# Kernel tuning notes

Measured on AMD Instinct MI355X. Metric: run time of the kernel, lower is better.

## Reference

```python
import jax, jax.numpy as jnp
import numpy as np

K = 20
EPS = 1e-5


def _bn(x, g, b):
    # inference-mode BatchNorm with running_mean=0, running_var=1 (fresh init)
    return x * (g / jnp.sqrt(1.0 + EPS)) + b


def _lrelu(x):
    return jax.nn.leaky_relu(x, 0.2)


def _knn(x, k):
    # x: [B,N,D] -> idx [B,N,k] of nearest neighbors (includes self)
    sq = jnp.sum(x * x, axis=-1)                       # [B,N]
    inner = jnp.einsum('bnd,bmd->bnm', x, x)           # [B,N,N]
    dist = sq[:, :, None] - 2.0 * inner + sq[:, None, :]
    _, idx = jax.lax.top_k(-dist, k)
    return idx


def _edge_feat(x, k):
    # x: [B,N,D] -> [B,N,k,2D] = concat(neighbor - center, center)
    idx = _knn(x, k)
    nbr = jax.vmap(lambda xb, ib: xb[ib])(x, idx)      # [B,N,k,D]
    ctr = jnp.broadcast_to(x[:, :, None, :], nbr.shape)
    return jnp.concatenate([nbr - ctr, ctr], axis=-1)


def _edge_conv(x, W, g, b, k):
    # conv1x1 (no bias) + BN + LeakyReLU + max over neighbors
    f = _edge_feat(x, k)                               # [B,N,k,2D]
    h = jnp.einsum('bnkc,oc->bnko', f, W)
    return jnp.max(_lrelu(_bn(h, g, b)), axis=2)       # [B,N,out]


def setup_inputs() -> dict:
    key = jax.random.key(0)
    ks = jax.random.split(key, 12)
    B, N = 8, 4096
    num_classes = 5
    r = lambda k_, shape: jax.random.normal(k_, shape, jnp.float32) * 0.1
    return {
        'xyz': jax.random.normal(ks[0], (B, N, 3), jnp.float32),
        'W1': r(ks[1], (64, 6)),   'g1': jnp.ones((64,), jnp.float32),  'b1': jnp.zeros((64,), jnp.float32),
        'W2': r(ks[2], (64, 128)), 'g2': jnp.ones((64,), jnp.float32),  'b2': jnp.zeros((64,), jnp.float32),
        'W3': r(ks[3], (64, 128)), 'g3': jnp.ones((64,), jnp.float32),  'b3': jnp.zeros((64,), jnp.float32),
        'W4': r(ks[4], (128, 128)),'g4': jnp.ones((128,), jnp.float32), 'b4': jnp.zeros((128,), jnp.float32),
        'W5': r(ks[5], (1024, 320)),'g5': jnp.ones((1024,), jnp.float32),'b5': jnp.zeros((1024,), jnp.float32),
        'Wl1': r(ks[6], (512, 2048)),'g6': jnp.ones((512,), jnp.float32),'b6': jnp.zeros((512,), jnp.float32),
        'Wl2': r(ks[7], (256, 512)), 'bl2': jnp.zeros((256,), jnp.float32),
        'g7': jnp.ones((256,), jnp.float32), 'b7': jnp.zeros((256,), jnp.float32),
        'Wl3': r(ks[8], (num_classes, 256)), 'bl3': jnp.zeros((num_classes,), jnp.float32),
    }


def reference(xyz, W1, g1, b1, W2, g2, b2, W3, g3, b3, W4, g4, b4,
              W5, g5, b5, Wl1, g6, b6, Wl2, bl2, g7, b7, Wl3, bl3):
    B, N, _ = xyz.shape
    k = min(K, N - 1)
    x1 = _edge_conv(xyz, W1, g1, b1, k)                # [B,N,64]
    x2 = _edge_conv(x1, W2, g2, b2, k)                 # [B,N,64]
    x3 = _edge_conv(x2, W3, g3, b3, k)                 # [B,N,64]
    x4 = _edge_conv(x3, W4, g4, b4, k)                 # [B,N,128]
    xc = jnp.concatenate([x1, x2, x3, x4], axis=-1)    # [B,N,320]
    h = _lrelu(_bn(jnp.einsum('bnc,oc->bno', xc, W5), g5, b5))  # [B,N,1024]
    gmax = jnp.max(h, axis=1)
    gavg = jnp.mean(h, axis=1)
    gfeat = jnp.concatenate([gmax, gavg], axis=-1)     # [B,2048]
    y = _lrelu(_bn(gfeat @ Wl1.T, g6, b6))             # dropout = identity (eval)
    y = _lrelu(_bn(y @ Wl2.T + bl2, g7, b7))
    y = y @ Wl3.T + bl3                                # [B,num_classes]
    return jnp.broadcast_to(y[:, None, :], (B, N, y.shape[-1]))
```

## Files before the change

kernel.cpp:

```cpp
#include <hip/hip_runtime.h>


constexpr int NB  = 8;
constexpr int NPT = 4096;
constexpr int KNB = 20;

typedef _Float16 half8 __attribute__((ext_vector_type(8)));
typedef float f32x4 __attribute__((ext_vector_type(4)));

__device__ __forceinline__ unsigned int fmono(float f) {
  unsigned int u = __float_as_uint(f);
  return u ^ ((unsigned int)(((int)u) >> 31) | 0x80000000u);
}

__device__ __attribute__((noinline)) unsigned long long sort_row(int row, int n,
                                                                 int lane) {
  extern __shared__ char smem[];
  unsigned long long* buf = (unsigned long long*)smem + (size_t)row * 64;
  const unsigned long long INFK = ~0ull;
  unsigned long long a = (lane < n) ? buf[lane] : INFK;
#pragma unroll
  for (int k = 2; k <= 64; k <<= 1) {
#pragma unroll
    for (int j = k >> 1; j > 0; j >>= 1) {
      const bool tm = (((lane & k) == 0) == ((lane & j) == 0));
      const unsigned long long oa = __shfl_xor(a, j, 64);
      a = ((a < oa) == tm) ? a : oa;
    }
  }
  if (lane < 20) buf[lane] = a;
  return a;
}

__device__ __forceinline__ void sel_q(unsigned long long key, int base_r,
                                      int quad, int l15, int lane,
                                      unsigned long long& tau_r, int& cnt_r) {
  extern __shared__ char smem[];
  unsigned long long* bufB = (unsigned long long*)smem;
  bool pass = key < tau_r;
  unsigned long long m = __ballot(pass);
  if (m == 0) return;
  unsigned int seg = (unsigned int)(m >> (quad * 16)) & 0xFFFFu;
  int pc = __popc(seg);
  const unsigned long long needm = __ballot(cnt_r + pc > 64);
  if (needm != 0) {
#pragma unroll
    for (int q = 0; q < 4; ++q) {
      if ((needm >> (q * 16)) & 1ull) {
        const int nq = __shfl(cnt_r, q * 16, 64);
        const unsigned long long sv = sort_row(base_r + q * 4, nq, lane);
        const unsigned long long t19 = __shfl(sv, 19, 64);
        if (quad == q) { tau_r = t19; cnt_r = 20; }
      }
    }
    pass = key < tau_r;
    m = __ballot(pass);
    seg = (unsigned int)(m >> (quad * 16)) & 0xFFFFu;
    pc = __popc(seg);
  }
  if (pass) {
    const int off = __popc(seg & ((1u << l15) - 1u));
    bufB[(size_t)(base_r + quad * 4) * 64 + cnt_r + off] = key;
  }
  cnt_r += pc;
}

__global__ __launch_bounds__(256) void cvt_xyz(const float* __restrict__ xyz,
                                               float* __restrict__ x0) {
  const int t = blockIdx.x * 256 + threadIdx.x;
  float4 v;
  v.x = xyz[t * 3 + 0];
  v.y = xyz[t * 3 + 1];
  v.z = xyz[t * 3 + 2];
  v.w = 0.0f;
  *(float4*)(x0 + (size_t)t * 4) = v;
}

__global__ __launch_bounds__(256) void sqsplit(const float* __restrict__ x,
                                               float* __restrict__ sqo,
                                               unsigned short* __restrict__ xhi,
                                               unsigned short* __restrict__ xlo) {
  const int t = blockIdx.x * 256 + threadIdx.x;
  const int p = t >> 2, c = t & 3;
  const float* src = x + (size_t)p * 64 + c * 16;
  float s = 0.0f;
  unsigned short hb[16], lb[16];
#pragma unroll
  for (int e = 0; e < 16; e += 4) {
    const float4 v = *(const float4*)(src + e);
    const float vv[4] = {v.x, v.y, v.z, v.w};
#pragma unroll
    for (int u = 0; u < 4; ++u) {
      const float f = vv[u];
      s = fmaf(f, f, s);
      const _Float16 h = (_Float16)f;
      const _Float16 l = (_Float16)(f - (float)h);
      hb[e + u] = __builtin_bit_cast(unsigned short, h);
      lb[e + u] = __builtin_bit_cast(unsigned short, l);
    }
  }
  unsigned short* dh = xhi + (size_t)p * 64 + c * 16;
  unsigned short* dl = xlo + (size_t)p * 64 + c * 16;
  *(uint4*)dh = *(uint4*)hb;
  *(uint4*)(dh + 8) = *(uint4*)(hb + 8);
  *(uint4*)dl = *(uint4*)lb;
  *(uint4*)(dl + 8) = *(uint4*)(lb + 8);
  s += __shfl_xor(s, 1, 64);
  s += __shfl_xor(s, 2, 64);
  if (c == 0) sqo[p] = s;
}

__global__ __launch_bounds__(256, 4) void knn3(const float* __restrict__ x0,
                                               int* __restrict__ idxout) {
  const int b = blockIdx.y, i0 = blockIdx.x * 64;
  const int tid = threadIdx.x, w = tid >> 6, lane = tid & 63;
  const int l15 = lane & 15, quad = lane >> 4;
  const float* xb = x0 + (size_t)b * (NPT * 4);

  float xix[4], xiy[4], xiz[4];
#pragma unroll
  for (int r = 0; r < 4; ++r) {
    const float4 v =
        *(const float4*)(xb + (size_t)(i0 + w * 16 + quad * 4 + r) * 4);
    xix[r] = v.x;
    xiy[r] = v.y;
    xiz[r] = v.z;
  }

  unsigned long long tau[4] = {~0ull, ~0ull, ~0ull, ~0ull};
  int cnt[4] = {0, 0, 0, 0};

  for (int jt = 0; jt < NPT / 64; ++jt) {
    const int j0 = jt * 64;
    float4 xj[4];
#pragma unroll
    for (int nj = 0; nj < 4; ++nj)
      xj[nj] = *(const float4*)(xb + (size_t)(j0 + nj * 16 + l15) * 4);
#pragma unroll
    for (int r = 0; r < 4; ++r) {
#pragma unroll
      for (int nj = 0; nj < 4; ++nj) {
        const float dx = xj[nj].x - xix[r];
        const float dy = xj[nj].y - xiy[r];
        const float dz = xj[nj].z - xiz[r];
        const float dd = fmaf(dx, dx, fmaf(dy, dy, dz * dz));
        const unsigned long long key =
            ((unsigned long long)fmono(dd) << 32) |
            (unsigned int)(j0 + nj * 16 + l15);
        sel_q(key, w * 16 + r, quad, l15, lane, tau[r], cnt[r]);
      }
    }
  }
#pragma unroll
  for (int rw = 0; rw < 16; ++rw) {
    const int q = rw >> 2, r = rw & 3;
    const int nq = __shfl(cnt[r], q * 16, 64);
    const unsigned long long sv = sort_row(w * 16 + rw, nq, lane);
    const int i = i0 + w * 16 + rw;
    if (lane < 20)
      idxout[((size_t)(b * NPT + i)) * KNB + lane] = (int)(unsigned int)sv;
  }
}

__global__ __launch_bounds__(256, 4) void knn_mfma(
    const unsigned short* __restrict__ xhi16,
    const unsigned short* __restrict__ xlo16,
    const float* __restrict__ sqn, int* __restrict__ idxout) {
  const int b = blockIdx.y, i0 = blockIdx.x * 64;
  const int tid = threadIdx.x, w = tid >> 6, lane = tid & 63;
  const int l15 = lane & 15, quad = lane >> 4;

  const half8* Hb = (const half8*)(xhi16 + (size_t)b * NPT * 64);
  const half8* Lb = (const half8*)(xlo16 + (size_t)b * NPT * 64);
  const float* sqb = sqn + b * NPT;

  const int ia = i0 + w * 16 + l15;
  const half8 ah0 = Hb[(size_t)ia * 8 + quad];
  const half8 ah1 = Hb[(size_t)ia * 8 + 4 + quad];
  const half8 al0 = Lb[(size_t)ia * 8 + quad];
  const half8 al1 = Lb[(size_t)ia * 8 + 4 + quad];

  unsigned long long tau[4] = {~0ull, ~0ull, ~0ull, ~0ull};
  int cnt[4] = {0, 0, 0, 0};

  for (int jt = 0; jt < NPT / 64; ++jt) {
    const int j0 = jt * 64;
    float sq4[4];
#pragma unroll
    for (int nj = 0; nj < 4; ++nj) sq4[nj] = sqb[j0 + nj * 16 + l15];
    f32x4 acc[4];
#pragma unroll
    for (int nj = 0; nj < 4; ++nj) {
      const int jb = j0 + nj * 16 + l15;
      const half8 bh0 = Hb[(size_t)jb * 8 + quad];
      const half8 bh1 = Hb[(size_t)jb * 8 + 4 + quad];
      const half8 bl0 = Lb[(size_t)jb * 8 + quad];
      const half8 bl1 = Lb[(size_t)jb * 8 + 4 + quad];
      f32x4 a = {0.0f, 0.0f, 0.0f, 0.0f};
      a = __builtin_amdgcn_mfma_f32_16x16x32_f16(al0, bh0, a, 0, 0, 0);
      a = __builtin_amdgcn_mfma_f32_16x16x32_f16(al1, bh1, a, 0, 0, 0);
      a = __builtin_amdgcn_mfma_f32_16x16x32_f16(ah0, bl0, a, 0, 0, 0);
      a = __builtin_amdgcn_mfma_f32_16x16x32_f16(ah1, bl1, a, 0, 0, 0);
      a = __builtin_amdgcn_mfma_f32_16x16x32_f16(ah0, bh0, a, 0, 0, 0);
      a = __builtin_amdgcn_mfma_f32_16x16x32_f16(ah1, bh1, a, 0, 0, 0);
      acc[nj] = a;
    }
#pragma unroll
    for (int r = 0; r < 4; ++r) {
#pragma unroll
      for (int nj = 0; nj < 4; ++nj) {
        const float dd = fmaf(-2.0f, acc[nj][r], sq4[nj]);
        const unsigned long long key =
            ((unsigned long long)fmono(dd) << 32) |
            (unsigned int)(j0 + nj * 16 + l15);
        sel_q(key, w * 16 + r, quad, l15, lane, tau[r], cnt[r]);
      }
    }
  }
#pragma unroll
  for (int rw = 0; rw < 16; ++rw) {
    const int q = rw >> 2, r = rw & 3;
    const int nq = __shfl(cnt[r], q * 16, 64);
    const unsigned long long sv = sort_row(w * 16 + rw, nq, lane);
    const int i = i0 + w * 16 + rw;
    if (lane < 20)
      idxout[((size_t)(b * NPT + i)) * KNB + lane] = (int)(unsigned int)sv;
  }
}

template <int DIN, int DS, int COUT>
__global__ __launch_bounds__(256) void edge_kernel(
    const float* __restrict__ x, const int* __restrict__ idx,
    const float* __restrict__ W, const float* __restrict__ g,
    const float* __restrict__ bia, float* __restrict__ out) {
  constexpr int CG = COUT / 64;
  const int lane = threadIdx.x & 63;
  const int wglob = blockIdx.x * 4 + (threadIdx.x >> 6);
  const int n_lin = __builtin_amdgcn_readfirstlane(wglob / CG);
  const int cg = __builtin_amdgcn_readfirstlane(wglob % CG);
  const int b = n_lin >> 12;
  const int n = n_lin & (NPT - 1);
  const int c = cg * 64 + lane;

  const float* wrow = W + (size_t)c * (2 * DIN);
  const float invs = 1.0f / sqrtf(1.0f + 1e-5f);
  const float s = g[c] * invs;
  const float bias = bia[c];

  const float* xb = x + (size_t)b * (NPT * DS);
  const float* xi = xb + (size_t)n * DS;

  float wa[DIN];
  float base = 0.0f;
  if constexpr (DIN == 3) {
    wa[0] = wrow[0]; wa[1] = wrow[1]; wa[2] = wrow[2];
    const float wb0 = wrow[3], wb1 = wrow[4], wb2 = wrow[5];
    const float4 vi = *(const float4*)xi;
    base = (wb0 - wa[0]) * vi.x + (wb1 - wa[1]) * vi.y + (wb2 - wa[2]) * vi.z;
  } else {
#pragma unroll
    for (int d0 = 0; d0 < DIN; d0 += 4) {
      const float4 w4 = *(const float4*)(wrow + d0);
      wa[d0 + 0] = w4.x; wa[d0 + 1] = w4.y; wa[d0 + 2] = w4.z; wa[d0 + 3] = w4.w;
    }
#pragma unroll
    for (int d0 = 0; d0 < DIN; d0 += 4) {
      const float4 wb4 = *(const float4*)(wrow + DIN + d0);
      const float4 v0 = *(const float4*)(xi + d0);
      base += (wb4.x - wa[d0 + 0]) * v0.x + (wb4.y - wa[d0 + 1]) * v0.y +
              (wb4.z - wa[d0 + 2]) * v0.z + (wb4.w - wa[d0 + 3]) * v0.w;
    }
  }
  base = s * base + bias;

  const int* ip = idx + (size_t)n_lin * KNB;
  float m = -3.0e38f;
  for (int k = 0; k < KNB; ++k) {
    const int j = __builtin_amdgcn_readfirstlane(ip[k]);
    const float* xj = xb + (size_t)j * DS;
    float acc = 0.0f;
    if constexpr (DIN == 3) {
      const float4 v = *(const float4*)xj;
      acc = wa[0] * v.x + wa[1] * v.y + wa[2] * v.z;
    } else {
#pragma unroll
      for (int d0 = 0; d0 < DIN; d0 += 8) {
        const float4 v0 = *(const float4*)(xj + d0);
        const float4 v1 = *(const float4*)(xj + d0 + 4);
        acc += wa[d0 + 0] * v0.x + wa[d0 + 1] * v0.y + wa[d0 + 2] * v0.z +
               wa[d0 + 3] * v0.w + wa[d0 + 4] * v1.x + wa[d0 + 5] * v1.y +
               wa[d0 + 6] * v1.z + wa[d0 + 7] * v1.w;
      }
    }
    float v = s * acc + base;
    v = v > 0.0f ? v : 0.2f * v;
    m = fmaxf(m, v);
  }
  out[(size_t)n_lin * COUT + c] = m;
}

__global__ __launch_bounds__(256) void conv5_kernel(
    const float* __restrict__ x1, const float* __restrict__ x2,
    const float* __restrict__ x3, const float* __restrict__ x4,
    const float* __restrict__ W5, const float* __restrict__ g5,
    const float* __restrict__ b5, float* __restrict__ pmax,
    float* __restrict__ psum) {
  __shared__ float xcT[320][32];
  __shared__ float wT[8][256];
  const int nb = blockIdx.x, cb = blockIdx.y, b = blockIdx.z;
  const int tid = threadIdx.x;
  const int n0 = nb * 32;

#pragma unroll
  for (int p = 0; p < 10; ++p) {
    const int q = tid + p * 256;
    const int nloc = q / 80;
    const int kg = (q % 80) * 4;
    const float* src;
    int koff;
    if (kg < 64)       { src = x1 + ((size_t)(b * NPT + n0 + nloc)) * 64;  koff = kg; }
    else if (kg < 128) { src = x2 + ((size_t)(b * NPT + n0 + nloc)) * 64;  koff = kg - 64; }
    else if (kg < 192) { src = x3 + ((size_t)(b * NPT + n0 + nloc)) * 64;  koff = kg - 128; }
    else               { src = x4 + ((size_t)(b * NPT + n0 + nloc)) * 128; koff = kg - 192; }
    const float4 v = *(const float4*)(src + koff);
    xcT[kg + 0][nloc] = v.x; xcT[kg + 1][nloc] = v.y;
    xcT[kg + 2][nloc] = v.z; xcT[kg + 3][nloc] = v.w;
  }

  const int cg = tid >> 2, ng = tid & 3;
  const int c0 = cg * 4, n0t = ng * 8;
  float acc[4][8];
#pragma unroll
  for (int r = 0; r < 4; ++r)
#pragma unroll
    for (int e = 0; e < 8; ++e) acc[r][e] = 0.0f;

  for (int kt = 0; kt < 40; ++kt) {
    __syncthreads();
    {
      const float* wsrc = W5 + (size_t)(cb * 256 + tid) * 320 + kt * 8;
      const float4 a = *(const float4*)wsrc;
      const float4 b4 = *(const float4*)(wsrc + 4);
      wT[0][tid] = a.x; wT[1][tid] = a.y; wT[2][tid] = a.z; wT[3][tid] = a.w;
      wT[4][tid] = b4.x; wT[5][tid] = b4.y; wT[6][tid] = b4.z; wT[7][tid] = b4.w;
    }
    __syncthreads();
#pragma unroll
    for (int kk = 0; kk < 8; ++kk) {
      const float4 w4 = *(const float4*)&wT[kk][c0];
      const float4 xa = *(const float4*)&xcT[kt * 8 + kk][n0t];
      const float4 xb4 = *(const float4*)&xcT[kt * 8 + kk][n0t + 4];
      const float wr[4] = {w4.x, w4.y, w4.z, w4.w};
      const float xr[8] = {xa.x, xa.y, xa.z, xa.w, xb4.x, xb4.y, xb4.z, xb4.w};
#pragma unroll
      for (int r = 0; r < 4; ++r)
#pragma unroll
        for (int e = 0; e < 8; ++e) acc[r][e] = fmaf(wr[r], xr[e], acc[r][e]);
    }
  }

  const float invs = 1.0f / sqrtf(1.0f + 1e-5f);
#pragma unroll
  for (int r = 0; r < 4; ++r) {
    const int cglob = cb * 256 + c0 + r;
    const float s = g5[cglob] * invs;
    const float bb = b5[cglob];
    float mx = -3.0e38f, sm = 0.0f;
#pragma unroll
    for (int e = 0; e < 8; ++e) {
      float v = fmaf(s, acc[r][e], bb);
      v = v > 0.0f ? v : 0.2f * v;
      mx = fmaxf(mx, v);
      sm += v;
    }
    mx = fmaxf(mx, __shfl_xor(mx, 1, 64));
    mx = fmaxf(mx, __shfl_xor(mx, 2, 64));
    sm += __shfl_xor(sm, 1, 64);
    sm += __shfl_xor(sm, 2, 64);
    if (ng == 0) {
      pmax[((size_t)b * 1024 + cglob) * 128 + nb] = mx;
      psum[((size_t)b * 1024 + cglob) * 128 + nb] = sm;
    }
  }
}

__global__ __launch_bounds__(256) void reduce5(const float* __restrict__ pmax,
                                               const float* __restrict__ psum,
                                               float* __restrict__ gfeat) {
  const int t = blockIdx.x * 256 + threadIdx.x;
  const int b = t >> 10, c = t & 1023;
  const float* pm = pmax + (size_t)t * 128;
  const float* ps = psum + (size_t)t * 128;
  float mx = -3.0e38f, sm = 0.0f;
  for (int i = 0; i < 128; i += 4) {
    const float4 v = *(const float4*)(pm + i);
    mx = fmaxf(mx, fmaxf(fmaxf(v.x, v.y), fmaxf(v.z, v.w)));
    const float4 u = *(const float4*)(ps + i);
    sm += (u.x + u.y) + (u.z + u.w);
  }
  gfeat[b * 2048 + c] = mx;
  gfeat[b * 2048 + 1024 + c] = sm * (1.0f / 4096.0f);
}

__global__ __launch_bounds__(256) void head1(const float* __restrict__ gfeat,
                                             const float* __restrict__ Wl1,
                                             const float* __restrict__ g6,
                                             const float* __restrict__ b6,
                                             float* __restrict__ y1g) {
  __shared__ float gf[2048];
  __shared__ float red[256];
  const int tid = threadIdx.x;
  const int cb = blockIdx.x, b = blockIdx.y;
  const float4* gsrc = (const float4*)(gfeat + b * 2048);
  for (int p = tid; p < 512; p += 256) ((float4*)gf)[p] = gsrc[p];
  __syncthreads();
  const int cl = cb * 64 + (tid >> 2);
  const int q = tid & 3;
  const float* wr = Wl1 + (size_t)cl * 2048 + q * 512;
  const float* gq = gf + q * 512;
  float acc = 0.0f;
  for (int k0 = 0; k0 < 512; k0 += 8) {
    const float4 w0 = *(const float4*)(wr + k0);
    const float4 w1 = *(const float4*)(wr + k0 + 4);
    acc = fmaf(w0.x, gq[k0 + 0], acc); acc = fmaf(w0.y, gq[k0 + 1], acc);
    acc = fmaf(w0.z, gq[k0 + 2], acc); acc = fmaf(w0.w, gq[k0 + 3], acc);
    acc = fmaf(w1.x, gq[k0 + 4], acc); acc = fmaf(w1.y, gq[k0 + 5], acc);
    acc = fmaf(w1.z, gq[k0 + 6], acc); acc = fmaf(w1.w, gq[k0 + 7], acc);
  }
  red[tid] = acc;
  __syncthreads();
  if (q == 0) {
    float v = red[tid] + red[tid + 1] + red[tid + 2] + red[tid + 3];
    const float invs = 1.0f / sqrtf(1.0f + 1e-5f);
    v = fmaf(g6[cl] * invs, v, b6[cl]);
    v = v > 0.0f ? v : 0.2f * v;
    y1g[b * 512 + cl] = v;
  }
}

__global__ __launch_bounds__(256) void head2(
    const float* __restrict__ y1g, const float* __restrict__ Wl2,
    const float* __restrict__ bl2, const float* __restrict__ g7,
    const float* __restrict__ b7, const float* __restrict__ Wl3,
    const float* __restrict__ bl3, float* __restrict__ out) {
  __shared__ float y1s[512];
  __shared__ float y2s[256];
  __shared__ float y3s[5];
  const int b = blockIdx.x;
  const int t = threadIdx.x;
  y1s[t] = y1g[b * 512 + t];
  y1s[t + 256] = y1g[b * 512 + t + 256];
  __syncthreads();
  {
    const float* wr = Wl2 + (size_t)t * 512;
    float acc = 0.0f;
    for (int k0 = 0; k0 < 512; k0 += 8) {
      const float4 w0 = *(const float4*)(wr + k0);
      const float4 w1 = *(const float4*)(wr + k0 + 4);
      acc = fmaf(w0.x, y1s[k0 + 0], acc); acc = fmaf(w0.y, y1s[k0 + 1], acc);
      acc = fmaf(w0.z, y1s[k0 + 2], acc); acc = fmaf(w0.w, y1s[k0 + 3], acc);
      acc = fmaf(w1.x, y1s[k0 + 4], acc); acc = fmaf(w1.y, y1s[k0 + 5], acc);
      acc = fmaf(w1.z, y1s[k0 + 6], acc); acc = fmaf(w1.w, y1s[k0 + 7], acc);
    }
    const float invs = 1.0f / sqrtf(1.0f + 1e-5f);
    float v = acc + bl2[t];
    v = fmaf(g7[t] * invs, v, b7[t]);
    v = v > 0.0f ? v : 0.2f * v;
    y2s[t] = v;
  }
  __syncthreads();
  if (t < 5) {
    const float* wr = Wl3 + (size_t)t * 256;
    float acc = 0.0f;
    for (int k = 0; k < 256; ++k) acc += wr[k] * y2s[k];
    y3s[t] = acc + bl3[t];
  }
  __syncthreads();
  for (int e = t; e < NPT * 5; e += 256)
    out[(size_t)b * (NPT * 5) + e] = y3s[e % 5];
}

extern "C" void kernel_launch(void* const* d_in, const int* in_sizes, int n_in,
                              void* d_out, int out_size, void* d_ws, size_t ws_size,
                              hipStream_t stream) {
  (void)in_sizes; (void)n_in; (void)out_size;
  const float* xyz = (const float*)d_in[0];
  const float* W1  = (const float*)d_in[1];
  const float* g1  = (const float*)d_in[2];
  const float* b1  = (const float*)d_in[3];
  const float* W2  = (const float*)d_in[4];
  const float* g2  = (const float*)d_in[5];
  const float* b2  = (const float*)d_in[6];
  const float* W3  = (const float*)d_in[7];
  const float* g3  = (const float*)d_in[8];
  const float* b3  = (const float*)d_in[9];
  const float* W4  = (const float*)d_in[10];
  const float* g4  = (const float*)d_in[11];
  const float* b4  = (const float*)d_in[12];
  const float* W5  = (const float*)d_in[13];
  const float* g5  = (const float*)d_in[14];
  const float* b5  = (const float*)d_in[15];
  const float* Wl1 = (const float*)d_in[16];
  const float* g6  = (const float*)d_in[17];
  const float* b6  = (const float*)d_in[18];
  const float* Wl2 = (const float*)d_in[19];
  const float* bl2 = (const float*)d_in[20];
  const float* g7  = (const float*)d_in[21];
  const float* b7  = (const float*)d_in[22];
  const float* Wl3 = (const float*)d_in[23];
  const float* bl3 = (const float*)d_in[24];

  char* ws = (char*)d_ws;
  float* x0    = (float*)(ws + 0);
  float* x1    = (float*)(ws + 524288);
  float* x2    = (float*)(ws + 8912896);
  float* x3    = (float*)(ws + 17301504);
  float* x4    = (float*)(ws + 25690112);
  float* sqb   = (float*)(ws + 42467328);
  int*   idxb  = (int*)  (ws + 42598400);
  float* pmx   = (float*)(ws + 45219840);
  float* psm   = (float*)(ws + 49414144);
  float* gfeat = (float*)(ws + 53608448);
  float* y1g   = (float*)(ws + 53673984);
  if (ws_size < 53690368) return;

  unsigned short* xhi = (unsigned short*)pmx;
  unsigned short* xlo = (unsigned short*)psm;

  cvt_xyz<<<128, 256, 0, stream>>>(xyz, x0);

  knn3<<<dim3(64, 8), 256, 32768, stream>>>(x0, idxb);
  edge_kernel<3, 4, 64><<<8192, 256, 0, stream>>>(x0, idxb, W1, g1, b1, x1);

  sqsplit<<<512, 256, 0, stream>>>(x1, sqb, xhi, xlo);
  knn_mfma<<<dim3(64, 8), 256, 32768, stream>>>(xhi, xlo, sqb, idxb);
  edge_kernel<64, 64, 64><<<8192, 256, 0, stream>>>(x1, idxb, W2, g2, b2, x2);

  sqsplit<<<512, 256, 0, stream>>>(x2, sqb, xhi, xlo);
  knn_mfma<<<dim3(64, 8), 256, 32768, stream>>>(xhi, xlo, sqb, idxb);
  edge_kernel<64, 64, 64><<<8192, 256, 0, stream>>>(x2, idxb, W3, g3, b3, x3);

  sqsplit<<<512, 256, 0, stream>>>(x3, sqb, xhi, xlo);
  knn_mfma<<<dim3(64, 8), 256, 32768, stream>>>(xhi, xlo, sqb, idxb);
  edge_kernel<64, 64, 128><<<16384, 256, 0, stream>>>(x3, idxb, W4, g4, b4, x4);

  conv5_kernel<<<dim3(128, 4, 8), 256, 0, stream>>>(x1, x2, x3, x4, W5, g5, b5, pmx, psm);
  reduce5<<<32, 256, 0, stream>>>(pmx, psm, gfeat);
  head1<<<dim3(8, 8), 256, 0, stream>>>(gfeat, Wl1, g6, b6, y1g);
  head2<<<8, 256, 0, stream>>>(y1g, Wl2, bl2, g7, b7, Wl3, bl3, (float*)d_out);
}
```

Before: 2.502 ms.

## Precompute per-point neighbor projection then gather instead of per-edge dot products

The edge convolution is split into two steps. A small GEMM kernel first computes Y = W_a·x_j once per point. A gather kernel then reads Y at each neighbor index and applies BN, LeakyReLU and the max. This removes the per-edge 64-wide dot product, which repeated the same work about 20 times, in exchange for extra launches and an intermediate buffer that reuses the pmx workspace. Conv4 is split into two 64-channel halves that run in sequence.

```diff
diff --git a/kernel.cpp b/kernel.cpp
--- a/kernel.cpp
+++ b/kernel.cpp
@@ -228,75 +228,109 @@
   }
 }
 
+__global__ __launch_bounds__(256) void featg3(const float* __restrict__ x0,
+                                              const float* __restrict__ W,
+                                              float* __restrict__ Y) {
+  const int lane = threadIdx.x & 63;
+  const int p0 = (blockIdx.x * 4 + (threadIdx.x >> 6)) * 4;
+  const float* wr = W + lane * 6;
+  const float w0 = wr[0], w1 = wr[1], w2 = wr[2];
+#pragma unroll
+  for (int r = 0; r < 4; ++r) {
+    const float4 v = *(const float4*)(x0 + (size_t)(p0 + r) * 4);
+    Y[(size_t)(p0 + r) * 64 + lane] = w0 * v.x + w1 * v.y + w2 * v.z;
+  }
+}
+
+__global__ __launch_bounds__(256) void featg64(const float* __restrict__ X,
+                                               const float* __restrict__ W,
+                                               int co, float* __restrict__ Y) {
+  __shared__ float Xt[64][68];
+  __shared__ float Wt[64][68];
+  const int tid = threadIdx.x;
+  const int n0 = blockIdx.x * 64;
+  const int pc = tid & 63, dg = tid >> 6;
+#pragma unroll
+  for (int rep = 0; rep < 4; ++rep) {
+    const int d0 = dg * 16 + rep * 4;
+    const float4 xv = *(const float4*)(X + (size_t)(n0 + pc) * 64 + d0);
+    Xt[d0 + 0][pc] = xv.x; Xt[d0 + 1][pc] = xv.y;
+    Xt[d0 + 2][pc] = xv.z; Xt[d0 + 3][pc] = xv.w;
+    const float4 wv = *(const float4*)(W + (size_t)(co + pc) * 128 + d0);
+    Wt[d0 + 0][pc] = wv.x; Wt[d0 + 1][pc] = wv.y;
+    Wt[d0 + 2][pc] = wv.z; Wt[d0 + 3][pc] = wv.w;
+  }
+  __syncthreads();
+  const int c0 = (tid & 15) * 4, p0 = (tid >> 4) * 4;
+  float acc[4][4];
+#pragma unroll
+  for (int i = 0; i < 4; ++i)
+#pragma unroll
+    for (int j = 0; j < 4; ++j) acc[i][j] = 0.0f;
+#pragma unroll 4
+  for (int d = 0; d < 64; ++d) {
+    const float4 xa = *(const float4*)&Xt[d][p0];
+    const float4 wc = *(const float4*)&Wt[d][c0];
+    const float xr[4] = {xa.x, xa.y, xa.z, xa.w};
+    const float wr[4] = {wc.x, wc.y, wc.z, wc.w};
+#pragma unroll
+    for (int i = 0; i < 4; ++i)
+#pragma unroll
+      for (int j = 0; j < 4; ++j) acc[i][j] = fmaf(xr[i], wr[j], acc[i][j]);
+  }
+#pragma unroll
+  for (int i = 0; i < 4; ++i) {
+    float4 o;
+    o.x = acc[i][0]; o.y = acc[i][1]; o.z = acc[i][2]; o.w = acc[i][3];
+    *(float4*)(Y + (size_t)(n0 + p0 + i) * 64 + c0) = o;
+  }
+}
+
 template <int DIN, int DS, int COUT>
-__global__ __launch_bounds__(256) void edge_kernel(
-    const float* __restrict__ x, const int* __restrict__ idx,
-    const float* __restrict__ W, const float* __restrict__ g,
-    const float* __restrict__ bia, float* __restrict__ out) {
-  constexpr int CG = COUT / 64;
+__global__ __launch_bounds__(256) void gather_edge(
+    const float* __restrict__ x, const float* __restrict__ Y,
+    const int* __restrict__ idx, const float* __restrict__ W,
+    const float* __restrict__ g, const float* __restrict__ bia,
+    float* __restrict__ out, int co) {
   const int lane = threadIdx.x & 63;
   const int wglob = blockIdx.x * 4 + (threadIdx.x >> 6);
-  const int n_lin = __builtin_amdgcn_readfirstlane(wglob / CG);
-  const int cg = __builtin_amdgcn_readfirstlane(wglob % CG);
-  const int b = n_lin >> 12;
-  const int n = n_lin & (NPT - 1);
-  const int c = cg * 64 + lane;
+  const int b = wglob >> 12;
+  const int c = co + lane;
 
   const float* wrow = W + (size_t)c * (2 * DIN);
+  const float* xi = x + (size_t)wglob * DS;
+  float Dv = 0.0f;
+  if constexpr (DIN == 3) {
+    const float4 v = *(const float4*)xi;
+    Dv = (wrow[3] - wrow[0]) * v.x + (wrow[4] - wrow[1]) * v.y +
+         (wrow[5] - wrow[2]) * v.z;
+  } else {
+#pragma unroll
+    for (int d0 = 0; d0 < DIN; d0 += 4) {
+      const float4 wa4 = *(const float4*)(wrow + d0);
+      const float4 wb4 = *(const float4*)(wrow + DIN + d0);
+      const float4 v = *(const float4*)(xi + d0);
+      Dv += (wb4.x - wa4.x) * v.x + (wb4.y - wa4.y) * v.y +
+            (wb4.z - wa4.z) * v.z + (wb4.w - wa4.w) * v.w;
+    }
+  }
   const float invs = 1.0f / sqrtf(1.0f + 1e-5f);
   const float s = g[c] * invs;
-  const float bias = bia[c];
-
-  const float* xb = x + (size_t)b * (NPT * DS);
-  const float* xi = xb + (size_t)n * DS;
-
-  float wa[DIN];
-  float base = 0.0f;
-  if constexpr (DIN == 3) {
-    wa[0] = wrow[0]; wa[1] = wrow[1]; wa[2] = wrow[2];
-    const float wb0 = wrow[3], wb1 = wrow[4], wb2 = wrow[5];
-    const float4 vi = *(const float4*)xi;
-    base = (wb0 - wa[0]) * vi.x + (wb1 - wa[1]) * vi.y + (wb2 - wa[2]) * vi.z;
-  } else {
-#pragma unroll
-    for (int d0 = 0; d0 < DIN; d0 += 4) {
-      const float4 w4 = *(const float4*)(wrow + d0);
-      wa[d0 + 0] = w4.x; wa[d0 + 1] = w4.y; wa[d0 + 2] = w4.z; wa[d0 + 3] = w4.w;
-    }
-#pragma unroll
-    for (int d0 = 0; d0 < DIN; d0 += 4) {
-      const float4 wb4 = *(const float4*)(wrow + DIN + d0);
-      const float4 v0 = *(const float4*)(xi + d0);
-      base += (wb4.x - wa[d0 + 0]) * v0.x + (wb4.y - wa[d0 + 1]) * v0.y +
-              (wb4.z - wa[d0 + 2]) * v0.z + (wb4.w - wa[d0 + 3]) * v0.w;
-    }
-  }
-  base = s * base + bias;
-
-  const int* ip = idx + (size_t)n_lin * KNB;
+  const float base = fmaf(s, Dv, bia[c]);
+
+  const int* ip = idx + (size_t)wglob * KNB;
+  const int jv = ip[lane < KNB ? lane : 0];
+  const float* Yb = Y + (((size_t)b) << 12) * 64;
   float m = -3.0e38f;
+#pragma unroll
   for (int k = 0; k < KNB; ++k) {
-    const int j = __builtin_amdgcn_readfirstlane(ip[k]);
-    const float* xj = xb + (size_t)j * DS;
-    float acc = 0.0f;
-    if constexpr (DIN == 3) {
-      const float4 v = *(const float4*)xj;
-      acc = wa[0] * v.x + wa[1] * v.y + wa[2] * v.z;
-    } else {
-#pragma unroll
-      for (int d0 = 0; d0 < DIN; d0 += 8) {
-        const float4 v0 = *(const float4*)(xj + d0);
-        const float4 v1 = *(const float4*)(xj + d0 + 4);
-        acc += wa[d0 + 0] * v0.x + wa[d0 + 1] * v0.y + wa[d0 + 2] * v0.z +
-               wa[d0 + 3] * v0.w + wa[d0 + 4] * v1.x + wa[d0 + 5] * v1.y +
-               wa[d0 + 6] * v1.z + wa[d0 + 7] * v1.w;
-      }
-    }
-    float v = s * acc + base;
+    const int j = __shfl(jv, k, 64);
+    const float yv = Yb[(size_t)j * 64 + lane];
+    float v = fmaf(s, yv, base);
     v = v > 0.0f ? v : 0.2f * v;
     m = fmaxf(m, v);
   }
-  out[(size_t)n_lin * COUT + c] = m;
+  out[(size_t)wglob * COUT + c] = m;
 }
 
 __global__ __launch_bounds__(256) void conv5_kernel(
@@ -526,23 +560,30 @@
 
   unsigned short* xhi = (unsigned short*)pmx;
   unsigned short* xlo = (unsigned short*)psm;
+  float* Yb = pmx;
 
   cvt_xyz<<<128, 256, 0, stream>>>(xyz, x0);
 
   knn3<<<dim3(64, 8), 256, 32768, stream>>>(x0, idxb);
-  edge_kernel<3, 4, 64><<<8192, 256, 0, stream>>>(x0, idxb, W1, g1, b1, x1);
+  featg3<<<2048, 256, 0, stream>>>(x0, W1, Yb);
+  gather_edge<3, 4, 64><<<8192, 256, 0, stream>>>(x0, Yb, idxb, W1, g1, b1, x1, 0);
 
   sqsplit<<<512, 256, 0, stream>>>(x1, sqb, xhi, xlo);
   knn_mfma<<<dim3(64, 8), 256, 32768, stream>>>(xhi, xlo, sqb, idxb);
-  edge_kernel<64, 64, 64><<<8192, 256, 0, stream>>>(x1, idxb, W2, g2, b2, x2);
+  featg64<<<512, 256, 0, stream>>>(x1, W2, 0, Yb);
+  gather_edge<64, 64, 64><<<8192, 256, 0, stream>>>(x1, Yb, idxb, W2, g2, b2, x2, 0);
 
   sqsplit<<<512, 256, 0, stream>>>(x2, sqb, xhi, xlo);
   knn_mfma<<<dim3(64, 8), 256, 32768, stream>>>(xhi, xlo, sqb, idxb);
-  edge_kernel<64, 64, 64><<<8192, 256, 0, stream>>>(x2, idxb, W3, g3, b3, x3);
+  featg64<<<512, 256, 0, stream>>>(x2, W3, 0, Yb);
+  gather_edge<64, 64, 64><<<8192, 256, 0, stream>>>(x2, Yb, idxb, W3, g3, b3, x3, 0);
 
   sqsplit<<<512, 256, 0, stream>>>(x3, sqb, xhi, xlo);
   knn_mfma<<<dim3(64, 8), 256, 32768, stream>>>(xhi, xlo, sqb, idxb);
-  edge_kernel<64, 64, 128><<<16384, 256, 0, stream>>>(x3, idxb, W4, g4, b4, x4);
+  featg64<<<512, 256, 0, stream>>>(x3, W4, 0, Yb);
+  gather_edge<64, 64, 128><<<8192, 256, 0, stream>>>(x3, Yb, idxb, W4, g4, b4, x4, 0);
+  featg64<<<512, 256, 0, stream>>>(x3, W4, 64, Yb);
+  gather_edge<64, 64, 128><<<8192, 256, 0, stream>>>(x3, Yb, idxb, W4, g4, b4, x4, 64);
 
   conv5_kernel<<<dim3(128, 4, 8), 256, 0, stream>>>(x1, x2, x3, x4, W5, g5, b5, pmx, psm);
   reduce5<<<32, 256, 0, stream>>>(pmx, psm, gfeat);
```

Measured after the change: 2.290 ms. 8.5% less time.
